# Kernel optimization log

Measured on AMD Instinct MI355X. Metric: run time of the kernel, lower is better.

## Reference

```python
import jax, jax.numpy as jnp
import numpy as np

M = 16    # manifold dim = latent_dim // 2
HID = 64  # metric MLP hidden width


def metric_single(x, W1, b1, W2, b2):
    """Metric tensor for a single point x: (m,) -> SPD (m, m)."""
    h = jnp.tanh(x @ W1 + b1)
    A = (h @ W2 + b2).reshape(M, M)
    return A @ A.T + jnp.eye(M, dtype=x.dtype)


def connection_coeffs(x, W1, b1, W2, b2):
    """Christoffel symbols Gamma^k_ab, shape (B, m, m, m)."""
    f = lambda xs: metric_single(xs, W1, b1, W2, b2)
    # partial_g[B, a, i, b] = d g_{ai} / d x_b
    partial_g = jax.vmap(jax.jacfwd(f))(x)
    g = jax.vmap(f)(x)                      # (B, m, m)
    inv_g = jnp.linalg.inv(g)               # small 16x16 inverses
    t1 = jnp.einsum('Bki,Baib->Bkab', inv_g, partial_g)
    t2 = jnp.einsum('Bki,Bbai->Bkab', inv_g, partial_g)
    t3 = jnp.einsum('Bki,Biab->Bkab', inv_g, partial_g)
    return 0.5 * (t1 + t2 - t3)


def geodesic_ode_f(z, W1, b1, W2, b2):
    """RHS of geodesic ODE; z = [x, v] of shape (B, 2m)."""
    x = z[:, :M]
    v = z[:, M:]
    Gamma = connection_coeffs(x, W1, b1, W2, b2)
    dv = -jnp.einsum('Bkab,Ba,Bb->Bk', Gamma, v, v)
    return jnp.concatenate([v, dv], axis=1)


def rk4_step(z, dt, f):
    k1 = f(z)
    k2 = f(z + 0.5 * dt * k1)
    k3 = f(z + 0.5 * dt * k2)
    k4 = f(z + dt * k3)
    return z + dt / 6.0 * (k1 + 2 * k2 + 2 * k3 + k4)


def setup_inputs() -> dict:
    key = jax.random.key(0)
    ks = jax.random.split(key, 5)
    B = 16384
    z = jax.random.normal(ks[0], (B, 2 * M), dtype=jnp.float32) * 0.5
    t = jnp.asarray(1.0, dtype=jnp.float32)
    W1 = jax.random.normal(ks[1], (M, HID), dtype=jnp.float32) * 0.3
    b1 = jax.random.normal(ks[2], (HID,), dtype=jnp.float32) * 0.1
    W2 = jax.random.normal(ks[3], (HID, M * M), dtype=jnp.float32) * 0.05
    b2 = jax.random.normal(ks[4], (M * M,), dtype=jnp.float32) * 0.05
    return {"z": z, "t": t, "W1": W1, "b1": b1, "W2": W2, "b2": b2, "num_steps": 4}


def reference(z, t, W1, b1, W2, b2, num_steps):
    """Geodesic exponential map exp(x0, v0, t) via num_steps RK4 steps."""
    dt = t / num_steps
    f = lambda zz: geodesic_ode_f(zz, W1, b1, W2, b2)
    for _ in range(num_steps):  # small fixed sequential loop (num_steps=4)
        z = rk4_step(z, dt, f)
    return z
```

## Files before the change

kernel.cpp:

```cpp
#include <hip/hip_runtime.h>
#include <math.h>


typedef _Float16 f16;
typedef _Float16 f16x2 __attribute__((ext_vector_type(2)));
typedef _Float16 f16x4 __attribute__((ext_vector_type(4)));
typedef _Float16 f16x8 __attribute__((ext_vector_type(8)));
typedef __fp16 h16x2 __attribute__((ext_vector_type(2)));
typedef float f32x2 __attribute__((ext_vector_type(2)));
typedef float f32x4 __attribute__((ext_vector_type(4)));
typedef float f32x16 __attribute__((ext_vector_type(16)));

#define SAG_P 392
#define SZ_P  36
#define SH_P  72
#define SW_P  20
#define SWP_C 20

__device__ __forceinline__ float fastTanh(float x) {
    float e = exp2f(x * 2.885390081777927f);
    return 1.0f - 2.0f * __builtin_amdgcn_rcpf(1.0f + e);
}

__device__ __forceinline__ f16x2 pk2(float a, float b) {
    h16x2 p = __builtin_amdgcn_cvt_pkrtz(a, b);
    return __builtin_bit_cast(f16x2, p);
}

typedef union { f16x4 v4; f16x2 v2[2]; } u16x4;
typedef union { f16x8 v8; f16x2 v2[4]; int i32[4]; } u16x8;

template<int K>
__device__ __forceinline__ float bcf(float x) {
    int v = __builtin_amdgcn_mov_dpp(__builtin_bit_cast(int, x),
                                     0x150 | K, 0xf, 0xf, false);
    return __builtin_bit_cast(float, v);
}

template<int K>
__device__ __forceinline__ void fe_all(float (&R)[17], const int i16, float &myinv) {
    if constexpr (K < 16) {
        float pvk = bcf<K>(R[K]);
        float pinv = __builtin_amdgcn_rcpf(pvk);
        if (i16 == K) myinv = pinv;
        float f = (i16 == K) ? 0.0f : R[K] * pinv;
        #pragma unroll
        for (int j = K + 1; j <= 16; ++j) {
            float pv = bcf<K>(R[j]);
            R[j] -= f * pv;
        }
        fe_all<K + 1>(R, i16, myinv);
    }
}

__global__ __launch_bounds__(256, 1)
void geo_kernel(const float* __restrict__ zin, const float* __restrict__ tg,
                const float* __restrict__ W1g, const float* __restrict__ b1g,
                const float* __restrict__ W2g, const float* __restrict__ b2g,
                const int* __restrict__ nsg, float* __restrict__ outg, int B)
{
    __shared__ __align__(16) f16   sAG[16 * SAG_P];
    __shared__ __align__(16) f16   sHT[16 * SH_P];
    __shared__ __align__(16) float sZI[16 * SZ_P];
    __shared__ __align__(16) float sKV[16 * SW_P];
    __shared__ __align__(16) float sWp[4 * 16 * SWP_C];

    const int tid = threadIdx.x;
    const int w = tid >> 6;
    const int l = tid & 63;
    const int i16 = l & 15, q4 = l >> 4, h2 = l >> 5, sc = q4 & 1;

    f16x8 w2a[4][2];
    #pragma unroll
    for (int t = 0; t < 4; ++t)
        #pragma unroll
        for (int ch = 0; ch < 2; ++ch)
            #pragma unroll
            for (int j = 0; j < 8; ++j)
                w2a[t][ch][j] = (f16)W2g[(8*q4 + j + 32*ch)*256 + i16 + 16*(4*w + t)];

    f16x8 w2r[8];
    #pragma unroll
    for (int ch = 0; ch < 8; ++ch)
        #pragma unroll
        for (int j = 0; j < 8; ++j)
            w2r[ch][j] = (f16)W2g[(i16 + 16*w)*256 + 8*q4 + j + 32*ch];

    f16x8 w1h;
    #pragma unroll
    for (int j = 0; j < 8; ++j) {
        int k = 8*q4 + j;
        w1h[j] = (k < 16) ? (f16)W1g[k*64 + i16 + 16*w] : (f16)0.0f;
    }

    f16x8 w1q[2];
    #pragma unroll
    for (int ch = 0; ch < 2; ++ch)
        #pragma unroll
        for (int j = 0; j < 8; ++j)
            w1q[ch][j] = (f16)W1g[i16*64 + 8*q4 + j + 32*ch];

    float b2v[4][4];
    #pragma unroll
    for (int t = 0; t < 4; ++t)
        #pragma unroll
        for (int reg = 0; reg < 4; ++reg)
            b2v[t][reg] = b2g[16*(4*w + t) + 4*q4 + reg];
    float b1v[4];
    #pragma unroll
    for (int reg = 0; reg < 4; ++reg) b1v[reg] = b1g[16*w + 4*q4 + reg];

    const int pb = blockIdx.x * 16;
    const int p_cmb = tid >> 4;
    const int g16 = tid & 15;
    f32x2 zc, ar;
    {
        int pg = (pb + p_cmb < B) ? (pb + p_cmb) : (B - 1);
        zc = *(const f32x2*)&zin[pg*32 + 2*g16];
        *(f32x2*)&sZI[p_cmb*SZ_P + 2*g16] = zc;
    }
    __syncthreads();

    const float tv = tg[0];
    const int nst = nsg[0];
    const float dt = tv / (float)nst;

    const int xmask = (q4 >= 2) ? 0 : -1;

    #pragma unroll 1
    for (int st = 0; st < nst; ++st) {
        #pragma unroll 1
        for (int s = 0; s < 4; ++s) {
            u16x8 xf;
            {
                f32x4 xa = *(const f32x4*)&sZI[i16*SZ_P + 8*sc];
                f32x4 xb = *(const f32x4*)&sZI[i16*SZ_P + 8*sc + 4];
                xf.v2[0] = pk2(xa[0], xa[1]);
                xf.v2[1] = pk2(xa[2], xa[3]);
                xf.v2[2] = pk2(xb[0], xb[1]);
                xf.v2[3] = pk2(xb[2], xb[3]);
                #pragma unroll
                for (int jp = 0; jp < 4; ++jp) xf.i32[jp] &= xmask;
            }
            float dreg[4];
            {
                f32x4 hc = {0.f, 0.f, 0.f, 0.f};
                hc = __builtin_amdgcn_mfma_f32_16x16x32_f16(w1h, xf.v8, hc, 0, 0, 0);
                float hv[4];
                #pragma unroll
                for (int reg = 0; reg < 4; ++reg) {
                    hv[reg] = fastTanh(hc[reg] + b1v[reg]);
                    dreg[reg] = hv[reg]*hv[reg] - 1.0f;
                }
                u16x4 hv4;
                hv4.v2[0] = pk2(hv[0], hv[1]);
                hv4.v2[1] = pk2(hv[2], hv[3]);
                *(f16x4*)&sHT[i16*SH_P + 16*w + 4*q4] = hv4.v4;
            }
            __syncthreads();
            {
                f32x4 vA = *(const f32x4*)&sZI[i16*SZ_P + 16 + 4*w];
                f16x8 hf0 = *(const f16x8*)&sHT[i16*SH_P + 8*q4];
                f16x8 hf1 = *(const f16x8*)&sHT[i16*SH_P + 8*q4 + 32];
                float pw[4] = {0.f, 0.f, 0.f, 0.f};
                #pragma unroll
                for (int t = 0; t < 4; ++t) {
                    f32x4 ac = {0.f, 0.f, 0.f, 0.f};
                    ac = __builtin_amdgcn_mfma_f32_16x16x32_f16(w2a[t][0], hf0, ac, 0, 0, 0);
                    ac = __builtin_amdgcn_mfma_f32_16x16x32_f16(w2a[t][1], hf1, ac, 0, 0, 0);
                    float a0 = ac[0] + b2v[t][0], a1 = ac[1] + b2v[t][1];
                    float a2 = ac[2] + b2v[t][2], a3 = ac[3] + b2v[t][3];
                    float vv = vA[t];
                    pw[0] += vv * a0; pw[1] += vv * a1;
                    pw[2] += vv * a2; pw[3] += vv * a3;
                    u16x4 av;
                    av.v2[0] = pk2(a0, a1);
                    av.v2[1] = pk2(a2, a3);
                    *(f16x4*)&sAG[i16*SAG_P + 24*(4*w + t) + 4*q4] = av.v4;
                }
                f32x4 pwv = {pw[0], pw[1], pw[2], pw[3]};
                *(f32x4*)&sWp[(w*16 + i16)*SWP_C + 4*q4] = pwv;
            }
            __syncthreads();
            #pragma unroll
            for (int u0 = 0; u0 < 2; ++u0) {
                int u = 2*w + u0;
                int pt = 2*u + sc;
                f16x8 af = *(const f16x8*)&sAG[pt*SAG_P + 24*i16 + 8*h2];
                f32x16 gz = {0.0f};
                f32x16 gacc = __builtin_amdgcn_mfma_f32_32x32x16_f16(af, af, gz, 0, 0, 0);
                float gv[8];
                #pragma unroll
                for (int rr = 0; rr < 4; ++rr) {
                    float lo0 = gacc[rr],     hi0 = gacc[rr + 8];
                    float lo1 = gacc[rr + 4], hi1 = gacc[rr + 12];
                    float g0 = sc ? hi0 : lo0;
                    float g1 = sc ? hi1 : lo1;
                    int a0 = 4*h2 + rr;
                    int a1 = 8 + 4*h2 + rr;
                    gv[rr]     = g0 + ((i16 == a0) ? 1.0f : 0.0f);
                    gv[4 + rr] = g1 + ((i16 == a1) ? 1.0f : 0.0f);
                }
                u16x4 g0p, g1p;
                g0p.v2[0] = pk2(gv[0], gv[1]); g0p.v2[1] = pk2(gv[2], gv[3]);
                g1p.v2[0] = pk2(gv[4], gv[5]); g1p.v2[1] = pk2(gv[6], gv[7]);
                *(f16x4*)&sAG[pt*SAG_P + 24*i16 + 4*h2]     = g0p.v4;
                *(f16x4*)&sAG[pt*SAG_P + 24*i16 + 8 + 4*h2] = g1p.v4;
            }
            {
                float vch[8];
                {
                    const float* vp = &sZI[i16*SZ_P + 16 + (q4 >> 1)];
                    #pragma unroll
                    for (int c = 0; c < 8; ++c) vch[c] = vp[2*c];
                }
                float wv[8];
                {
                    f32x4 s0 = *(const f32x4*)&sWp[(0*16 + i16)*SWP_C + 8*sc];
                    f32x4 s1 = *(const f32x4*)&sWp[(1*16 + i16)*SWP_C + 8*sc];
                    f32x4 s2 = *(const f32x4*)&sWp[(2*16 + i16)*SWP_C + 8*sc];
                    f32x4 s3 = *(const f32x4*)&sWp[(3*16 + i16)*SWP_C + 8*sc];
                    f32x4 t0 = *(const f32x4*)&sWp[(0*16 + i16)*SWP_C + 8*sc + 4];
                    f32x4 t1 = *(const f32x4*)&sWp[(1*16 + i16)*SWP_C + 8*sc + 4];
                    f32x4 t2 = *(const f32x4*)&sWp[(2*16 + i16)*SWP_C + 8*sc + 4];
                    f32x4 t3 = *(const f32x4*)&sWp[(3*16 + i16)*SWP_C + 8*sc + 4];
                    #pragma unroll
                    for (int j = 0; j < 4; ++j) {
                        wv[j]     = s0[j] + s1[j] + s2[j] + s3[j];
                        wv[4 + j] = t0[j] + t1[j] + t2[j] + t3[j];
                    }
                }
                f16x2 wfp[4];
                #pragma unroll
                for (int jp = 0; jp < 4; ++jp) wfp[jp] = pk2(wv[2*jp], wv[2*jp + 1]);
                f32x4 racc = {0.f, 0.f, 0.f, 0.f};
                #pragma unroll
                for (int ch = 0; ch < 8; ++ch) {
                    f16 vvh = (f16)vch[ch];
                    f16x2 vv2; vv2.x = vvh; vv2.y = vvh;
                    u16x8 uf;
                    #pragma unroll
                    for (int jp = 0; jp < 4; ++jp) uf.v2[jp] = vv2 * wfp[jp];
                    racc = __builtin_amdgcn_mfma_f32_16x16x32_f16(w2r[ch], uf.v8, racc, 0, 0, 0);
                }
                u16x4 tv4;
                tv4.v2[0] = pk2(dreg[0]*racc[0], dreg[1]*racc[1]);
                tv4.v2[1] = pk2(dreg[2]*racc[2], dreg[3]*racc[3]);
                *(f16x4*)&sHT[i16*SH_P + 16*w + 4*q4] = tv4.v4;
            }
            __syncthreads();
            {
                int ptq = 4*w + (i16 & 3);
                f16x8 tb0 = *(const f16x8*)&sHT[ptq*SH_P + 8*q4];
                f16x8 tb1 = *(const f16x8*)&sHT[ptq*SH_P + 8*q4 + 32];
                f32x4 qa = {0.f, 0.f, 0.f, 0.f};
                qa = __builtin_amdgcn_mfma_f32_16x16x32_f16(w1q[0], tb0, qa, 0, 0, 0);
                qa = __builtin_amdgcn_mfma_f32_16x16x32_f16(w1q[1], tb1, qa, 0, 0, 0);
                if (i16 < 4) {
                    #pragma unroll
                    for (int reg = 0; reg < 4; ++reg)
                        sAG[(4*w + i16)*SAG_P + 24*(4*q4 + reg) + 16] = (f16)qa[reg];
                }
            }
            {
                const int psl = 4*w + q4;
                float R[17];
                {
                    const f16* rp = &sAG[psl*SAG_P + 24*i16];
                    f16x8 ra = *(const f16x8*)&rp[0];
                    f16x8 rb = *(const f16x8*)&rp[8];
                    #pragma unroll
                    for (int j = 0; j < 8; ++j) { R[j] = (float)ra[j]; R[8+j] = (float)rb[j]; }
                    R[16] = (float)rp[16];
                }
                float myinv = 1.0f;
                fe_all<0>(R, i16, myinv);
                sKV[psl*SW_P + i16] = R[16] * myinv;
            }
            {
                f32x2 kk;
                if (g16 < 8) kk = *(const f32x2*)&sZI[p_cmb*SZ_P + 16 + 2*g16];
                else         kk = *(const f32x2*)&sKV[p_cmb*SW_P + 2*(g16 - 8)];
                if (s == 0) ar = kk;
                else {
                    float wgt = (s == 3) ? 1.0f : 2.0f;
                    ar.x += wgt * kk.x; ar.y += wgt * kk.y;
                }
                f32x2 zi;
                if (s < 3) {
                    float alpha = (s < 2) ? (0.5f * dt) : dt;
                    zi.x = zc.x + alpha * kk.x; zi.y = zc.y + alpha * kk.y;
                } else {
                    float c6 = dt / 6.0f;
                    zc.x += c6 * ar.x; zc.y += c6 * ar.y;
                    zi = zc;
                }
                *(f32x2*)&sZI[p_cmb*SZ_P + 2*g16] = zi;
            }
            __syncthreads();
        }
    }
    if (pb + p_cmb < B)
        *(f32x2*)&outg[(pb + p_cmb)*32 + 2*g16] = zc;
}

extern "C" void kernel_launch(void* const* d_in, const int* in_sizes, int n_in,
                              void* d_out, int out_size, void* d_ws, size_t ws_size,
                              hipStream_t stream) {
    (void)n_in; (void)d_ws; (void)ws_size; (void)out_size;
    const float* z  = (const float*)d_in[0];
    const float* t  = (const float*)d_in[1];
    const float* W1 = (const float*)d_in[2];
    const float* b1 = (const float*)d_in[3];
    const float* W2 = (const float*)d_in[4];
    const float* b2 = (const float*)d_in[5];
    const int*   ns = (const int*)d_in[6];
    float* out = (float*)d_out;
    const int B = in_sizes[0] / 32;
    int grid = (B + 15) / 16;
    hipLaunchKernelGGL(geo_kernel, dim3(grid), dim3(256), 0, stream,
                       z, t, W1, b1, W2, b2, ns, out, B);
}
```

Before: 171.5 us.

## Process two 16-point groups per block to interleave independent work

Each block now handles 32 points as two independent 16-point groups. Every stage runs over both groups between the same barriers, and the Gauss elimination runs two interleaved systems at once. The goal is more instruction-level parallelism for MFMA, DPP and rcp latency chains, and fewer barriers per point, with half as many blocks. In exchange it doubles LDS and register use, which could hurt occupancy or cause spills under launch_bounds(256,1), and the grid shrinks to 512 blocks.

```diff
diff --git a/kernel.cpp b/kernel.cpp
--- a/kernel.cpp
+++ b/kernel.cpp
@@ -38,18 +38,24 @@
 }
 
 template<int K>
-__device__ __forceinline__ void fe_all(float (&R)[17], const int i16, float &myinv) {
+__device__ __forceinline__ void fe_all2(float (&R0)[17], float (&R1)[17],
+                                        const int i16, float &inv0, float &inv1) {
     if constexpr (K < 16) {
-        float pvk = bcf<K>(R[K]);
-        float pinv = __builtin_amdgcn_rcpf(pvk);
-        if (i16 == K) myinv = pinv;
-        float f = (i16 == K) ? 0.0f : R[K] * pinv;
+        float p0 = bcf<K>(R0[K]);
+        float p1 = bcf<K>(R1[K]);
+        float pi0 = __builtin_amdgcn_rcpf(p0);
+        float pi1 = __builtin_amdgcn_rcpf(p1);
+        if (i16 == K) { inv0 = pi0; inv1 = pi1; }
+        float f0 = (i16 == K) ? 0.0f : R0[K] * pi0;
+        float f1 = (i16 == K) ? 0.0f : R1[K] * pi1;
         #pragma unroll
         for (int j = K + 1; j <= 16; ++j) {
-            float pv = bcf<K>(R[j]);
-            R[j] -= f * pv;
+            float v0 = bcf<K>(R0[j]);
+            float v1 = bcf<K>(R1[j]);
+            R0[j] -= f0 * v0;
+            R1[j] -= f1 * v1;
         }
-        fe_all<K + 1>(R, i16, myinv);
+        fe_all2<K + 1>(R0, R1, i16, inv0, inv1);
     }
 }
 
@@ -59,11 +65,11 @@
                 const float* __restrict__ W2g, const float* __restrict__ b2g,
                 const int* __restrict__ nsg, float* __restrict__ outg, int B)
 {
-    __shared__ __align__(16) f16   sAG[16 * SAG_P];
-    __shared__ __align__(16) f16   sHT[16 * SH_P];
-    __shared__ __align__(16) float sZI[16 * SZ_P];
-    __shared__ __align__(16) float sKV[16 * SW_P];
-    __shared__ __align__(16) float sWp[4 * 16 * SWP_C];
+    __shared__ __align__(16) f16   sAG[2][16 * SAG_P];
+    __shared__ __align__(16) f16   sHT[2][16 * SH_P];
+    __shared__ __align__(16) float sZI[2][16 * SZ_P];
+    __shared__ __align__(16) float sKV[2][16 * SW_P];
+    __shared__ __align__(16) float sWp[2][4 * 16 * SWP_C];
 
     const int tid = threadIdx.x;
     const int w = tid >> 6;
@@ -110,14 +116,16 @@
     #pragma unroll
     for (int reg = 0; reg < 4; ++reg) b1v[reg] = b1g[16*w + 4*q4 + reg];
 
-    const int pb = blockIdx.x * 16;
+    const int pb = blockIdx.x * 32;
     const int p_cmb = tid >> 4;
     const int g16 = tid & 15;
-    f32x2 zc, ar;
-    {
-        int pg = (pb + p_cmb < B) ? (pb + p_cmb) : (B - 1);
-        zc = *(const f32x2*)&zin[pg*32 + 2*g16];
-        *(f32x2*)&sZI[p_cmb*SZ_P + 2*g16] = zc;
+    f32x2 zc[2], ar[2];
+    #pragma unroll
+    for (int g = 0; g < 2; ++g) {
+        int pl = pb + 16*g + p_cmb;
+        int pg = (pl < B) ? pl : (B - 1);
+        zc[g] = *(const f32x2*)&zin[pg*32 + 2*g16];
+        *(f32x2*)&sZI[g][p_cmb*SZ_P + 2*g16] = zc[g];
     }
     __syncthreads();
 
@@ -131,37 +139,39 @@
     for (int st = 0; st < nst; ++st) {
         #pragma unroll 1
         for (int s = 0; s < 4; ++s) {
-            u16x8 xf;
-            {
-                f32x4 xa = *(const f32x4*)&sZI[i16*SZ_P + 8*sc];
-                f32x4 xb = *(const f32x4*)&sZI[i16*SZ_P + 8*sc + 4];
-                xf.v2[0] = pk2(xa[0], xa[1]);
-                xf.v2[1] = pk2(xa[2], xa[3]);
-                xf.v2[2] = pk2(xb[0], xb[1]);
-                xf.v2[3] = pk2(xb[2], xb[3]);
-                #pragma unroll
-                for (int jp = 0; jp < 4; ++jp) xf.i32[jp] &= xmask;
-            }
-            float dreg[4];
-            {
+            float dreg[2][4];
+            #pragma unroll
+            for (int g = 0; g < 2; ++g) {
+                u16x8 xf;
+                {
+                    f32x4 xa = *(const f32x4*)&sZI[g][i16*SZ_P + 8*sc];
+                    f32x4 xb = *(const f32x4*)&sZI[g][i16*SZ_P + 8*sc + 4];
+                    xf.v2[0] = pk2(xa[0], xa[1]);
+                    xf.v2[1] = pk2(xa[2], xa[3]);
+                    xf.v2[2] = pk2(xb[0], xb[1]);
+                    xf.v2[3] = pk2(xb[2], xb[3]);
+                    #pragma unroll
+                    for (int jp = 0; jp < 4; ++jp) xf.i32[jp] &= xmask;
+                }
                 f32x4 hc = {0.f, 0.f, 0.f, 0.f};
                 hc = __builtin_amdgcn_mfma_f32_16x16x32_f16(w1h, xf.v8, hc, 0, 0, 0);
                 float hv[4];
                 #pragma unroll
                 for (int reg = 0; reg < 4; ++reg) {
                     hv[reg] = fastTanh(hc[reg] + b1v[reg]);
-                    dreg[reg] = hv[reg]*hv[reg] - 1.0f;
+                    dreg[g][reg] = hv[reg]*hv[reg] - 1.0f;
                 }
                 u16x4 hv4;
                 hv4.v2[0] = pk2(hv[0], hv[1]);
                 hv4.v2[1] = pk2(hv[2], hv[3]);
-                *(f16x4*)&sHT[i16*SH_P + 16*w + 4*q4] = hv4.v4;
+                *(f16x4*)&sHT[g][i16*SH_P + 16*w + 4*q4] = hv4.v4;
             }
             __syncthreads();
-            {
-                f32x4 vA = *(const f32x4*)&sZI[i16*SZ_P + 16 + 4*w];
-                f16x8 hf0 = *(const f16x8*)&sHT[i16*SH_P + 8*q4];
-                f16x8 hf1 = *(const f16x8*)&sHT[i16*SH_P + 8*q4 + 32];
+            #pragma unroll
+            for (int g = 0; g < 2; ++g) {
+                f32x4 vA = *(const f32x4*)&sZI[g][i16*SZ_P + 16 + 4*w];
+                f16x8 hf0 = *(const f16x8*)&sHT[g][i16*SH_P + 8*q4];
+                f16x8 hf1 = *(const f16x8*)&sHT[g][i16*SH_P + 8*q4 + 32];
                 float pw[4] = {0.f, 0.f, 0.f, 0.f};
                 #pragma unroll
                 for (int t = 0; t < 4; ++t) {
@@ -176,54 +186,58 @@
                     u16x4 av;
                     av.v2[0] = pk2(a0, a1);
                     av.v2[1] = pk2(a2, a3);
-                    *(f16x4*)&sAG[i16*SAG_P + 24*(4*w + t) + 4*q4] = av.v4;
+                    *(f16x4*)&sAG[g][i16*SAG_P + 24*(4*w + t) + 4*q4] = av.v4;
                 }
                 f32x4 pwv = {pw[0], pw[1], pw[2], pw[3]};
-                *(f32x4*)&sWp[(w*16 + i16)*SWP_C + 4*q4] = pwv;
+                *(f32x4*)&sWp[g][(w*16 + i16)*SWP_C + 4*q4] = pwv;
             }
             __syncthreads();
             #pragma unroll
-            for (int u0 = 0; u0 < 2; ++u0) {
-                int u = 2*w + u0;
-                int pt = 2*u + sc;
-                f16x8 af = *(const f16x8*)&sAG[pt*SAG_P + 24*i16 + 8*h2];
-                f32x16 gz = {0.0f};
-                f32x16 gacc = __builtin_amdgcn_mfma_f32_32x32x16_f16(af, af, gz, 0, 0, 0);
-                float gv[8];
-                #pragma unroll
-                for (int rr = 0; rr < 4; ++rr) {
-                    float lo0 = gacc[rr],     hi0 = gacc[rr + 8];
-                    float lo1 = gacc[rr + 4], hi1 = gacc[rr + 12];
-                    float g0 = sc ? hi0 : lo0;
-                    float g1 = sc ? hi1 : lo1;
-                    int a0 = 4*h2 + rr;
-                    int a1 = 8 + 4*h2 + rr;
-                    gv[rr]     = g0 + ((i16 == a0) ? 1.0f : 0.0f);
-                    gv[4 + rr] = g1 + ((i16 == a1) ? 1.0f : 0.0f);
-                }
-                u16x4 g0p, g1p;
-                g0p.v2[0] = pk2(gv[0], gv[1]); g0p.v2[1] = pk2(gv[2], gv[3]);
-                g1p.v2[0] = pk2(gv[4], gv[5]); g1p.v2[1] = pk2(gv[6], gv[7]);
-                *(f16x4*)&sAG[pt*SAG_P + 24*i16 + 4*h2]     = g0p.v4;
-                *(f16x4*)&sAG[pt*SAG_P + 24*i16 + 8 + 4*h2] = g1p.v4;
-            }
-            {
+            for (int g = 0; g < 2; ++g) {
+                #pragma unroll
+                for (int u0 = 0; u0 < 2; ++u0) {
+                    int u = 2*w + u0;
+                    int pt = 2*u + sc;
+                    f16x8 af = *(const f16x8*)&sAG[g][pt*SAG_P + 24*i16 + 8*h2];
+                    f32x16 gz = {0.0f};
+                    f32x16 gacc = __builtin_amdgcn_mfma_f32_32x32x16_f16(af, af, gz, 0, 0, 0);
+                    float gv[8];
+                    #pragma unroll
+                    for (int rr = 0; rr < 4; ++rr) {
+                        float lo0 = gacc[rr],     hi0 = gacc[rr + 8];
+                        float lo1 = gacc[rr + 4], hi1 = gacc[rr + 12];
+                        float g0 = sc ? hi0 : lo0;
+                        float g1 = sc ? hi1 : lo1;
+                        int a0 = 4*h2 + rr;
+                        int a1 = 8 + 4*h2 + rr;
+                        gv[rr]     = g0 + ((i16 == a0) ? 1.0f : 0.0f);
+                        gv[4 + rr] = g1 + ((i16 == a1) ? 1.0f : 0.0f);
+                    }
+                    u16x4 g0p, g1p;
+                    g0p.v2[0] = pk2(gv[0], gv[1]); g0p.v2[1] = pk2(gv[2], gv[3]);
+                    g1p.v2[0] = pk2(gv[4], gv[5]); g1p.v2[1] = pk2(gv[6], gv[7]);
+                    *(f16x4*)&sAG[g][pt*SAG_P + 24*i16 + 4*h2]     = g0p.v4;
+                    *(f16x4*)&sAG[g][pt*SAG_P + 24*i16 + 8 + 4*h2] = g1p.v4;
+                }
+            }
+            #pragma unroll
+            for (int g = 0; g < 2; ++g) {
                 float vch[8];
                 {
-                    const float* vp = &sZI[i16*SZ_P + 16 + (q4 >> 1)];
+                    const float* vp = &sZI[g][i16*SZ_P + 16 + (q4 >> 1)];
                     #pragma unroll
                     for (int c = 0; c < 8; ++c) vch[c] = vp[2*c];
                 }
                 float wv[8];
                 {
-                    f32x4 s0 = *(const f32x4*)&sWp[(0*16 + i16)*SWP_C + 8*sc];
-                    f32x4 s1 = *(const f32x4*)&sWp[(1*16 + i16)*SWP_C + 8*sc];
-                    f32x4 s2 = *(const f32x4*)&sWp[(2*16 + i16)*SWP_C + 8*sc];
-                    f32x4 s3 = *(const f32x4*)&sWp[(3*16 + i16)*SWP_C + 8*sc];
-                    f32x4 t0 = *(const f32x4*)&sWp[(0*16 + i16)*SWP_C + 8*sc + 4];
-                    f32x4 t1 = *(const f32x4*)&sWp[(1*16 + i16)*SWP_C + 8*sc + 4];
-                    f32x4 t2 = *(const f32x4*)&sWp[(2*16 + i16)*SWP_C + 8*sc + 4];
-                    f32x4 t3 = *(const f32x4*)&sWp[(3*16 + i16)*SWP_C + 8*sc + 4];
+                    f32x4 s0 = *(const f32x4*)&sWp[g][(0*16 + i16)*SWP_C + 8*sc];
+                    f32x4 s1 = *(const f32x4*)&sWp[g][(1*16 + i16)*SWP_C + 8*sc];
+                    f32x4 s2 = *(const f32x4*)&sWp[g][(2*16 + i16)*SWP_C + 8*sc];
+                    f32x4 s3 = *(const f32x4*)&sWp[g][(3*16 + i16)*SWP_C + 8*sc];
+                    f32x4 t0 = *(const f32x4*)&sWp[g][(0*16 + i16)*SWP_C + 8*sc + 4];
+                    f32x4 t1 = *(const f32x4*)&sWp[g][(1*16 + i16)*SWP_C + 8*sc + 4];
+                    f32x4 t2 = *(const f32x4*)&sWp[g][(2*16 + i16)*SWP_C + 8*sc + 4];
+                    f32x4 t3 = *(const f32x4*)&sWp[g][(3*16 + i16)*SWP_C + 8*sc + 4];
                     #pragma unroll
                     for (int j = 0; j < 4; ++j) {
                         wv[j]     = s0[j] + s1[j] + s2[j] + s3[j];
@@ -244,64 +258,78 @@
                     racc = __builtin_amdgcn_mfma_f32_16x16x32_f16(w2r[ch], uf.v8, racc, 0, 0, 0);
                 }
                 u16x4 tv4;
-                tv4.v2[0] = pk2(dreg[0]*racc[0], dreg[1]*racc[1]);
-                tv4.v2[1] = pk2(dreg[2]*racc[2], dreg[3]*racc[3]);
-                *(f16x4*)&sHT[i16*SH_P + 16*w + 4*q4] = tv4.v4;
+                tv4.v2[0] = pk2(dreg[g][0]*racc[0], dreg[g][1]*racc[1]);
+                tv4.v2[1] = pk2(dreg[g][2]*racc[2], dreg[g][3]*racc[3]);
+                *(f16x4*)&sHT[g][i16*SH_P + 16*w + 4*q4] = tv4.v4;
             }
             __syncthreads();
-            {
+            #pragma unroll
+            for (int g = 0; g < 2; ++g) {
                 int ptq = 4*w + (i16 & 3);
-                f16x8 tb0 = *(const f16x8*)&sHT[ptq*SH_P + 8*q4];
-                f16x8 tb1 = *(const f16x8*)&sHT[ptq*SH_P + 8*q4 + 32];
+                f16x8 tb0 = *(const f16x8*)&sHT[g][ptq*SH_P + 8*q4];
+                f16x8 tb1 = *(const f16x8*)&sHT[g][ptq*SH_P + 8*q4 + 32];
                 f32x4 qa = {0.f, 0.f, 0.f, 0.f};
                 qa = __builtin_amdgcn_mfma_f32_16x16x32_f16(w1q[0], tb0, qa, 0, 0, 0);
                 qa = __builtin_amdgcn_mfma_f32_16x16x32_f16(w1q[1], tb1, qa, 0, 0, 0);
                 if (i16 < 4) {
                     #pragma unroll
                     for (int reg = 0; reg < 4; ++reg)
-                        sAG[(4*w + i16)*SAG_P + 24*(4*q4 + reg) + 16] = (f16)qa[reg];
+                        sAG[g][(4*w + i16)*SAG_P + 24*(4*q4 + reg) + 16] = (f16)qa[reg];
                 }
             }
             {
                 const int psl = 4*w + q4;
-                float R[17];
+                float R0[17], R1[17];
                 {
-                    const f16* rp = &sAG[psl*SAG_P + 24*i16];
-                    f16x8 ra = *(const f16x8*)&rp[0];
-                    f16x8 rb = *(const f16x8*)&rp[8];
-                    #pragma unroll
-                    for (int j = 0; j < 8; ++j) { R[j] = (float)ra[j]; R[8+j] = (float)rb[j]; }
-                    R[16] = (float)rp[16];
-                }
-                float myinv = 1.0f;
-                fe_all<0>(R, i16, myinv);
-                sKV[psl*SW_P + i16] = R[16] * myinv;
-            }
-            {
+                    const f16* rp0 = &sAG[0][psl*SAG_P + 24*i16];
+                    const f16* rp1 = &sAG[1][psl*SAG_P + 24*i16];
+                    f16x8 ra0 = *(const f16x8*)&rp0[0];
+                    f16x8 rb0 = *(const f16x8*)&rp0[8];
+                    f16x8 ra1 = *(const f16x8*)&rp1[0];
+                    f16x8 rb1 = *(const f16x8*)&rp1[8];
+                    #pragma unroll
+                    for (int j = 0; j < 8; ++j) {
+                        R0[j] = (float)ra0[j]; R0[8+j] = (float)rb0[j];
+                        R1[j] = (float)ra1[j]; R1[8+j] = (float)rb1[j];
+                    }
+                    R0[16] = (float)rp0[16];
+                    R1[16] = (float)rp1[16];
+                }
+                float inv0 = 1.0f, inv1 = 1.0f;
+                fe_all2<0>(R0, R1, i16, inv0, inv1);
+                sKV[0][psl*SW_P + i16] = R0[16] * inv0;
+                sKV[1][psl*SW_P + i16] = R1[16] * inv1;
+            }
+            #pragma unroll
+            for (int g = 0; g < 2; ++g) {
                 f32x2 kk;
-                if (g16 < 8) kk = *(const f32x2*)&sZI[p_cmb*SZ_P + 16 + 2*g16];
-                else         kk = *(const f32x2*)&sKV[p_cmb*SW_P + 2*(g16 - 8)];
-                if (s == 0) ar = kk;
+                if (g16 < 8) kk = *(const f32x2*)&sZI[g][p_cmb*SZ_P + 16 + 2*g16];
+                else         kk = *(const f32x2*)&sKV[g][p_cmb*SW_P + 2*(g16 - 8)];
+                if (s == 0) ar[g] = kk;
                 else {
                     float wgt = (s == 3) ? 1.0f : 2.0f;
-                    ar.x += wgt * kk.x; ar.y += wgt * kk.y;
+                    ar[g].x += wgt * kk.x; ar[g].y += wgt * kk.y;
                 }
                 f32x2 zi;
                 if (s < 3) {
                     float alpha = (s < 2) ? (0.5f * dt) : dt;
-                    zi.x = zc.x + alpha * kk.x; zi.y = zc.y + alpha * kk.y;
+                    zi.x = zc[g].x + alpha * kk.x; zi.y = zc[g].y + alpha * kk.y;
                 } else {
                     float c6 = dt / 6.0f;
-                    zc.x += c6 * ar.x; zc.y += c6 * ar.y;
-                    zi = zc;
-                }
-                *(f32x2*)&sZI[p_cmb*SZ_P + 2*g16] = zi;
+                    zc[g].x += c6 * ar[g].x; zc[g].y += c6 * ar[g].y;
+                    zi = zc[g];
+                }
+                *(f32x2*)&sZI[g][p_cmb*SZ_P + 2*g16] = zi;
             }
             __syncthreads();
         }
     }
-    if (pb + p_cmb < B)
-        *(f32x2*)&outg[(pb + p_cmb)*32 + 2*g16] = zc;
+    #pragma unroll
+    for (int g = 0; g < 2; ++g) {
+        int pl = pb + 16*g + p_cmb;
+        if (pl < B)
+            *(f32x2*)&outg[pl*32 + 2*g16] = zc[g];
+    }
 }
 
 extern "C" void kernel_launch(void* const* d_in, const int* in_sizes, int n_in,
@@ -317,7 +345,7 @@
     const int*   ns = (const int*)d_in[6];
     float* out = (float*)d_out;
     const int B = in_sizes[0] / 32;
-    int grid = (B + 15) / 16;
+    int grid = (B + 31) / 32;
     hipLaunchKernelGGL(geo_kernel, dim3(grid), dim3(256), 0, stream,
                        z, t, W1, b1, W2, b2, ns, out, B);
 }
```

New measurement: 168.6 us. Within noise of the previous version (-1.7%).
